# Kernel tuning notes

Hardware: AMD Instinct MI355X
Metric: run time of the kernel (lower is better)

## Reference

```python
import jax, jax.numpy as jnp
import numpy as np
import math

HIDDEN = 1024
HEADS = 16
HEAD_DIM = HIDDEN // HEADS
B, S = 2, 2048


def _xavier(key, shape):
    fan_in, fan_out = shape[1], shape[0]
    limit = math.sqrt(6.0 / (fan_in + fan_out))
    return jax.random.uniform(key, shape, jnp.float32, -limit, limit)


def setup_inputs() -> dict:
    key = jax.random.key(0)
    ks = jax.random.split(key, 5)
    x = jax.random.normal(ks[0], (B, S, HIDDEN), jnp.float32)
    # torch Linear stores weight as [out, in]; y = x @ W.T + b
    Wq = _xavier(ks[1], (HIDDEN, HIDDEN))
    Wk = _xavier(ks[2], (HIDDEN, HIDDEN))
    Wv = _xavier(ks[3], (HIDDEN, HIDDEN))
    Wo = _xavier(ks[4], (HIDDEN, HIDDEN))
    bq = jnp.zeros((HIDDEN,), jnp.float32)
    bk = jnp.zeros((HIDDEN,), jnp.float32)
    bv = jnp.zeros((HIDDEN,), jnp.float32)
    bo = jnp.zeros((HIDDEN,), jnp.float32)
    return {"x": x, "Wq": Wq, "bq": bq, "Wk": Wk, "bk": bk,
            "Wv": Wv, "bv": bv, "Wo": Wo, "bo": bo}


def reference(x, Wq, bq, Wk, bk, Wv, bv, Wo, bo):
    b, s, d = x.shape
    h, hd = HEADS, HEAD_DIM
    q = (x @ Wq.T + bq).reshape(b, s, h, hd).transpose(0, 2, 1, 3)  # [b,h,s,hd]
    k = (x @ Wk.T + bk).reshape(b, s, h, hd).transpose(0, 2, 1, 3)
    v = (x @ Wv.T + bv).reshape(b, s, h, hd).transpose(0, 2, 1, 3)
    scores = jnp.einsum('bhqd,bhkd->bhqk', q, k) / math.sqrt(hd)
    causal = jnp.tril(jnp.ones((s, s), bool))
    scores = jnp.where(causal, scores, -jnp.inf)
    attn = jax.nn.softmax(scores, axis=-1)
    out = jnp.einsum('bhqk,bhkd->bhqd', attn, v)  # [b,h,s,hd]
    out = out.transpose(0, 2, 1, 3).reshape(b, s, d)
    return out @ Wo.T + bo
```

## Files before the change

### kernel.cpp

```cpp
#include <hip/hip_runtime.h>
#include <hip/hip_bf16.h>


typedef __hip_bfloat16 bf16;
typedef __attribute__((ext_vector_type(8))) short short8;
typedef __attribute__((ext_vector_type(4))) short short4v;
typedef __attribute__((ext_vector_type(4))) float f32x4;
typedef __attribute__((ext_vector_type(2))) unsigned uint2v;
typedef __attribute__((ext_vector_type(4))) unsigned uint4v;

#define MFMA16(a, b, c) __builtin_amdgcn_mfma_f32_16x16x32_bf16((a), (b), (c), 0, 0, 0)

__device__ __forceinline__ void load_lds16(const void* g, void* l) {
  __builtin_amdgcn_global_load_lds(
      (const __attribute__((address_space(1))) void*)g,
      (__attribute__((address_space(3))) void*)l, 16, 0, 0);
}

#define QSCALE 0.18033688f

__global__ __launch_bounds__(256) void cvt_kernel(
    const float* __restrict__ x, const float* __restrict__ wq,
    const float* __restrict__ wk, const float* __restrict__ wv,
    const float* __restrict__ wo, bf16* __restrict__ xb,
    bf16* __restrict__ wcat) {
  const int bx = blockIdx.x;
  const float* src;
  bf16* dst;
  int ib;
  if (bx < 4096) { src = x; dst = xb; ib = bx; }
  else {
    const int wseg = (bx - 4096) >> 10;
    ib = (bx - 4096) & 1023;
    src = wseg == 0 ? wq : wseg == 1 ? wk : wseg == 2 ? wv : wo;
    dst = wcat + (size_t)wseg * 1048576;
  }
  const int i = (ib * 256 + threadIdx.x) * 4;
  const float4 v = *(const float4*)(src + i);
  short4v p;
  *(__hip_bfloat162*)&p = __float22bfloat162_rn(float2{v.x, v.y});
  *((__hip_bfloat162*)&p + 1) = __float22bfloat162_rn(float2{v.z, v.w});
  *(short4v*)(dst + i) = p;
}

__global__ __launch_bounds__(256) void qkv_kernel(
    const bf16* __restrict__ x, const bf16* __restrict__ Wcat,
    const float* __restrict__ bq, const float* __restrict__ bk,
    const float* __restrict__ bv, bf16* __restrict__ Qb,
    bf16* __restrict__ Kb, bf16* __restrict__ Vtg) {
  constexpr int K = 1024;
  __shared__ bf16 As[128 * 64];
  __shared__ bf16 Bs[128 * 64];
  const int t = threadIdx.x;
  const int lane = t & 63, w = t >> 6;
  const int quad = lane >> 4, r = lane & 15;
  const int bid = blockIdx.x;
  const int xcd = bid & 7, idx = bid >> 3;
  const int nloc = idx % 3, my = idx / 3;
  const int nx = xcd * 3 + nloc;
  const int m0 = my * 128;
  const int ncol = nx * 128;
  const int seg = ncol >> 10;
  const int n0 = ncol & 1023;
  const int wm = w >> 1, wn = w & 1;

  f32x4 acc[4][4] = {};

  for (int k0 = 0; k0 < K; k0 += 64) {
    __syncthreads();
#pragma unroll
    for (int p = 0; p < 4; ++p) {
      const int c = p * 256 + w * 64 + lane;
      const int row = c >> 3;
      const int scb = (c & 7) ^ (row & 7);
      load_lds16(x + (size_t)(m0 + row) * K + k0 + scb * 8, As + c * 8);
    }
#pragma unroll
    for (int p = 0; p < 4; ++p) {
      const int c = p * 256 + w * 64 + lane;
      const int row = c >> 3;
      const int scb = (c & 7) ^ (row & 7);
      load_lds16(Wcat + (size_t)(ncol + row) * K + k0 + scb * 8, Bs + c * 8);
    }
    __syncthreads();
    short8 af[4][2], bfr[4][2];
#pragma unroll
    for (int ks = 0; ks < 2; ++ks) {
#pragma unroll
      for (int i = 0; i < 4; ++i) {
        const int ra = wm * 64 + i * 16 + r;
        af[i][ks] = *(const short8*)(As + ra * 64 +
                                     (((ks * 4 + quad) ^ (ra & 7)) * 8));
        const int rb = wn * 64 + i * 16 + r;
        bfr[i][ks] = *(const short8*)(Bs + rb * 64 +
                                      (((ks * 4 + quad) ^ (rb & 7)) * 8));
      }
    }
#pragma unroll
    for (int ks = 0; ks < 2; ++ks)
#pragma unroll
      for (int i = 0; i < 4; ++i)
#pragma unroll
        for (int j = 0; j < 4; ++j)
          acc[i][j] = MFMA16(af[i][ks], bfr[j][ks], acc[i][j]);
  }

  const float* bias = seg == 0 ? bq : seg == 1 ? bk : bv;
  const float scale = seg == 0 ? QSCALE : 1.0f;
  bf16* dst01 = seg == 0 ? Qb : Kb;
#pragma unroll
  for (int i = 0; i < 4; ++i) {
    const int m = m0 + wm * 64 + i * 16 + quad * 4;
#pragma unroll
    for (int j = 0; j < 4; ++j) {
      const int nn = n0 + wn * 64 + j * 16 + r;
      const float bv_ = bias[nn];
      if (seg == 2) {
        short4v pk;
        *(__hip_bfloat162*)&pk = __float22bfloat162_rn(
            float2{acc[i][j][0] + bv_, acc[i][j][1] + bv_});
        *((__hip_bfloat162*)&pk + 1) = __float22bfloat162_rn(
            float2{acc[i][j][2] + bv_, acc[i][j][3] + bv_});
        *(short4v*)(Vtg + (size_t)nn * 4096 + m) = pk;
      } else {
#pragma unroll
        for (int g = 0; g < 4; ++g)
          dst01[(size_t)(m + g) * 1024 + nn] =
              __float2bfloat16((acc[i][j][g] + bv_) * scale);
      }
    }
  }
}

__global__ __launch_bounds__(256) void proj_kernel(const bf16* __restrict__ X,
                                                   const bf16* __restrict__ W,
                                                   const float* __restrict__ bias,
                                                   float* __restrict__ Y) {
  constexpr int K = 1024, N = 1024;
  __shared__ bf16 As[64 * 64];
  __shared__ bf16 Bs[128 * 64];
  const int t = threadIdx.x;
  const int lane = t & 63, w = t >> 6;
  const int quad = lane >> 4, r = lane & 15;
  const int bid = blockIdx.x;
  const int xcd = bid & 7, idx = bid >> 3;
  const int m0 = idx * 64, n0 = xcd * 128;
  const int wm = w >> 1, wn = w & 1;

  f32x4 acc[2][4] = {};

  for (int k0 = 0; k0 < K; k0 += 64) {
    __syncthreads();
#pragma unroll
    for (int p = 0; p < 2; ++p) {
      const int c = p * 256 + w * 64 + lane;
      const int row = c >> 3;
      const int scb = (c & 7) ^ (row & 7);
      load_lds16(X + (size_t)(m0 + row) * K + k0 + scb * 8, As + c * 8);
    }
#pragma unroll
    for (int p = 0; p < 4; ++p) {
      const int c = p * 256 + w * 64 + lane;
      const int row = c >> 3;
      const int scb = (c & 7) ^ (row & 7);
      load_lds16(W + (size_t)(n0 + row) * K + k0 + scb * 8, Bs + c * 8);
    }
    __syncthreads();
    short8 af[2][2], bfr[4][2];
#pragma unroll
    for (int ks = 0; ks < 2; ++ks) {
#pragma unroll
      for (int i = 0; i < 2; ++i) {
        const int ra = wm * 32 + i * 16 + r;
        af[i][ks] = *(const short8*)(As + ra * 64 +
                                     (((ks * 4 + quad) ^ (ra & 7)) * 8));
      }
#pragma unroll
      for (int j = 0; j < 4; ++j) {
        const int rb = wn * 64 + j * 16 + r;
        bfr[j][ks] = *(const short8*)(Bs + rb * 64 +
                                      (((ks * 4 + quad) ^ (rb & 7)) * 8));
      }
    }
#pragma unroll
    for (int ks = 0; ks < 2; ++ks)
#pragma unroll
      for (int i = 0; i < 2; ++i)
#pragma unroll
        for (int j = 0; j < 4; ++j)
          acc[i][j] = MFMA16(af[i][ks], bfr[j][ks], acc[i][j]);
  }
#pragma unroll
  for (int i = 0; i < 2; ++i) {
    const int m = m0 + wm * 32 + i * 16 + quad * 4;
#pragma unroll
    for (int j = 0; j < 4; ++j) {
      const int n = n0 + wn * 64 + j * 16 + r;
      const float bv = bias[n];
#pragma unroll
      for (int g = 0; g < 4; ++g)
        Y[(size_t)(m + g) * N + n] = acc[i][j][g] + bv;
    }
  }
}

__global__ __launch_bounds__(256, 4) void attn_kernel(const bf16* __restrict__ Qb,
                                                      const bf16* __restrict__ Kb,
                                                      const bf16* __restrict__ Vtg,
                                                      bf16* __restrict__ Ob) {
  const int bid = blockIdx.x;
  const int x = bid & 7, u = (bid >> 3) & 31, k = bid >> 8;
  const int g = x + 8 * k;
  const int h = g & 15, b = g >> 4;
  const int u8 = (u + 8) & 31;
  const int j = (k == 0) ? u : (k == 1) ? 31 - u : (k == 2) ? u8 : 31 - u8;
  const int T = j + 1;

  const int t = threadIdx.x;
  const int lane = t & 63, w = t >> 6;
  const int qs = w & 1, kst = w >> 1;
  const int quad = lane >> 4, r = lane & 15;

  __shared__ __align__(16) bf16 smem[16384];

  const bf16 *kg[2], *vg[2];
  int lofs[2];
#pragma unroll
  for (int p = 0; p < 2; ++p) {
    const int c = p * 256 + t;
    const int row = c >> 3, scb = (c & 7) ^ (row & 7);
    kg[p] = Kb + (size_t)(b * 2048 + row) * 1024 + h * 64 + scb * 8;
    vg[p] = Vtg + (size_t)(h * 64 + row) * 4096 + (size_t)b * 2048 + scb * 8;
    lofs[p] = c * 8;
  }

  auto stage_tile = [&](int tile, int slot) {
    bf16* const kd = smem + slot * 4096;
    bf16* const vd = smem + 8192 + slot * 4096;
#pragma unroll
    for (int p = 0; p < 2; ++p)
      load_lds16(kg[p] + (size_t)tile * 65536, kd + lofs[p]);
#pragma unroll
    for (int p = 0; p < 2; ++p)
      load_lds16(vg[p] + tile * 64, vd + lofs[p]);
  };

  short8 qf[2][2];
#pragma unroll
  for (int qfr = 0; qfr < 2; ++qfr)
#pragma unroll
    for (int ks = 0; ks < 2; ++ks)
      qf[qfr][ks] = *(const short8*)(
          Qb + (size_t)(b * 2048 + j * 64 + qs * 32 + qfr * 16 + r) * 1024 +
          h * 64 + ks * 32 + quad * 8);

  f32x4 o[4][2] = {};
  float lsum[2] = {0.f, 0.f};

  stage_tile(0, 0);
  for (int s = 0; s < T; ++s) {
    if (s + 1 < T) {
      stage_tile(s + 1, (s + 1) & 1);
      asm volatile("s_waitcnt vmcnt(4)" ::: "memory");
    } else {
      asm volatile("s_waitcnt vmcnt(0)" ::: "memory");
    }
    __builtin_amdgcn_s_barrier();
    __builtin_amdgcn_sched_barrier(0);

    const bf16* const ksb = smem + (s & 1) * 4096;
    const bf16* const vtb = smem + 8192 + (s & 1) * 4096;

    __builtin_amdgcn_s_setprio(1);
    short8 kf[2][2];
#pragma unroll
    for (int mt2 = 0; mt2 < 2; ++mt2) {
      const int krow = kst * 32 + mt2 * 16 + r;
#pragma unroll
      for (int ks = 0; ks < 2; ++ks)
        kf[mt2][ks] = *(const short8*)(ksb + krow * 64 +
                                       (((ks * 4 + quad) ^ (r & 7)) * 8));
    }
    f32x4 st[2][2] = {};
#pragma unroll
    for (int mt2 = 0; mt2 < 2; ++mt2)
#pragma unroll
      for (int qfr = 0; qfr < 2; ++qfr) {
        st[mt2][qfr] = MFMA16(kf[mt2][0], qf[qfr][0], st[mt2][qfr]);
        st[mt2][qfr] = MFMA16(kf[mt2][1], qf[qfr][1], st[mt2][qfr]);
      }
    if (s == T - 1) {
#pragma unroll
      for (int mt2 = 0; mt2 < 2; ++mt2)
#pragma unroll
        for (int qfr = 0; qfr < 2; ++qfr) {
          const int kb2 = s * 64 + kst * 32 + mt2 * 16 + quad * 4;
          const int qrow = j * 64 + qs * 32 + qfr * 16 + r;
#pragma unroll
          for (int g4 = 0; g4 < 4; ++g4)
            if (kb2 + g4 > qrow) st[mt2][qfr][g4] = -1e30f;
        }
    }
    unsigned cpk[2][2][2];
#pragma unroll
    for (int mt2 = 0; mt2 < 2; ++mt2)
#pragma unroll
      for (int qfr = 0; qfr < 2; ++qfr) {
        const float p0 = __builtin_amdgcn_exp2f(st[mt2][qfr][0]);
        const float p1 = __builtin_amdgcn_exp2f(st[mt2][qfr][1]);
        const float p2 = __builtin_amdgcn_exp2f(st[mt2][qfr][2]);
        const float p3 = __builtin_amdgcn_exp2f(st[mt2][qfr][3]);
        lsum[qfr] += (p0 + p1) + (p2 + p3);
        unsigned u0, u1;
        *(__hip_bfloat162*)&u0 = __float22bfloat162_rn(float2{p0, p1});
        *(__hip_bfloat162*)&u1 = __float22bfloat162_rn(float2{p2, p3});
        cpk[mt2][qfr][0] = u0;
        cpk[mt2][qfr][1] = u1;
      }
    short8 pf[2];
#pragma unroll
    for (int qfr = 0; qfr < 2; ++qfr) {
      unsigned br[4];
#pragma unroll
      for (int p2 = 0; p2 < 2; ++p2) {
        uint2v s32 = __builtin_amdgcn_permlane32_swap(
            cpk[0][qfr][p2], cpk[1][qfr][p2], false, false);
        uint2v s16 = __builtin_amdgcn_permlane16_swap(s32.x, s32.y,
                                                      false, false);
        br[p2] = s16.x; br[p2 + 2] = s16.y;
      }
      uint4v pv_; pv_.x = br[0]; pv_.y = br[1]; pv_.z = br[2]; pv_.w = br[3];
      pf[qfr] = __builtin_bit_cast(short8, pv_);
    }
#pragma unroll
    for (int mt = 0; mt < 4; ++mt) {
      const short8 vf = *(const short8*)(vtb + (mt * 16 + r) * 64 +
                                         (((kst * 4 + quad) ^ (r & 7)) * 8));
#pragma unroll
      for (int qfr = 0; qfr < 2; ++qfr)
        o[mt][qfr] = MFMA16(vf, pf[qfr], o[mt][qfr]);
    }
    __builtin_amdgcn_s_setprio(0);
    __builtin_amdgcn_sched_barrier(0);
    __builtin_amdgcn_s_barrier();
  }

#pragma unroll
  for (int qfr = 0; qfr < 2; ++qfr) {
    lsum[qfr] += __shfl_xor(lsum[qfr], 16);
    lsum[qfr] += __shfl_xor(lsum[qfr], 32);
  }
  __syncthreads();
  f32x4* const cb = (f32x4*)smem;
  float* const lb = (float*)(smem + 8192);
  if (kst == 1) {
#pragma unroll
    for (int mt = 0; mt < 4; ++mt)
#pragma unroll
      for (int qfr = 0; qfr < 2; ++qfr)
        cb[((qs * 2 + qfr) * 4 + mt) * 64 + lane] = o[mt][qfr];
#pragma unroll
    for (int qfr = 0; qfr < 2; ++qfr)
      lb[(qs * 2 + qfr) * 64 + lane] = lsum[qfr];
  }
  __syncthreads();
  if (kst == 0) {
    float inv[2];
#pragma unroll
    for (int qfr = 0; qfr < 2; ++qfr)
      inv[qfr] = 1.f / (lsum[qfr] + lb[(qs * 2 + qfr) * 64 + lane]);
#pragma unroll
    for (int mt = 0; mt < 4; ++mt)
#pragma unroll
      for (int qfr = 0; qfr < 2; ++qfr) {
        const f32x4 a = cb[((qs * 2 + qfr) * 4 + mt) * 64 + lane];
        short4v ph;
        *(__hip_bfloat162*)&ph = __float22bfloat162_rn(
            float2{(o[mt][qfr][0] + a[0]) * inv[qfr],
                   (o[mt][qfr][1] + a[1]) * inv[qfr]});
        *((__hip_bfloat162*)&ph + 1) = __float22bfloat162_rn(
            float2{(o[mt][qfr][2] + a[2]) * inv[qfr],
                   (o[mt][qfr][3] + a[3]) * inv[qfr]});
        *(short4v*)(Ob +
            (size_t)(b * 2048 + j * 64 + qs * 32 + qfr * 16 + r) * 1024 +
            h * 64 + mt * 16 + quad * 4) = ph;
      }
  }
}

extern "C" void kernel_launch(void* const* d_in, const int* in_sizes, int n_in,
                              void* d_out, int out_size, void* d_ws, size_t ws_size,
                              hipStream_t stream) {
  const float* x  = (const float*)d_in[0];
  const float* Wq = (const float*)d_in[1];
  const float* bq = (const float*)d_in[2];
  const float* Wk = (const float*)d_in[3];
  const float* bk = (const float*)d_in[4];
  const float* Wv = (const float*)d_in[5];
  const float* bv = (const float*)d_in[6];
  const float* Wo = (const float*)d_in[7];
  const float* bo = (const float*)d_in[8];
  float* out = (float*)d_out;

  bf16* xb   = (bf16*)d_ws;
  bf16* wcat = xb + (size_t)4096 * 1024;
  bf16* wob  = wcat + (size_t)3 * 1024 * 1024;
  bf16* Qb   = wcat + (size_t)4 * 1024 * 1024;
  bf16* Kb   = Qb  + (size_t)4096 * 1024;
  bf16* Vtg  = Kb  + (size_t)4096 * 1024;
  bf16* Ob   = Vtg + (size_t)4096 * 1024;
  const size_t need = ((size_t)4096 * 1024 * 5 + (size_t)1024 * 1024 * 4) * 2;
  if (ws_size < need) return;

  cvt_kernel<<<8192, 256, 0, stream>>>(x, Wq, Wk, Wv, Wo, xb, wcat);
  qkv_kernel<<<768, 256, 0, stream>>>(xb, wcat, bq, bk, bv, Qb, Kb, Vtg);
  attn_kernel<<<1024, 256, 0, stream>>>(Qb, Kb, Vtg, Ob);
  proj_kernel<<<512, 256, 0, stream>>>(Ob, wob, bo, out);
}
```

Baseline: 167.7 us.

## Restructure attention into single-wave blocks loading K/V straight to registers

The attention kernel drops its 4-wave blocks, which shared K/V tiles through double-buffered LDS and merged a split-K reduction at the end. It now launches 2048 one-wave blocks, each handling 32 query rows over the full 64-key tile. K and V fragments are loaded from global memory directly into registers with software double-buffering. This removes LDS staging, barriers and the cross-wave reduction, but each wave now fetches K/V on its own, which raises global/L2 traffic and register pressure.

```diff
diff --git a/kernel.cpp b/kernel.cpp
--- a/kernel.cpp
+++ b/kernel.cpp
@@ -204,86 +204,62 @@
   }
 }
 
-__global__ __launch_bounds__(256, 4) void attn_kernel(const bf16* __restrict__ Qb,
-                                                      const bf16* __restrict__ Kb,
-                                                      const bf16* __restrict__ Vtg,
-                                                      bf16* __restrict__ Ob) {
+__global__ __launch_bounds__(64, 2) void attn_kernel(const bf16* __restrict__ Qb,
+                                                     const bf16* __restrict__ Kb,
+                                                     const bf16* __restrict__ Vtg,
+                                                     bf16* __restrict__ Ob) {
   const int bid = blockIdx.x;
   const int x = bid & 7, u = (bid >> 3) & 31, k = bid >> 8;
-  const int g = x + 8 * k;
+  const int kk = k & 3, qh = k >> 2;
+  const int g = x + 8 * kk;
   const int h = g & 15, b = g >> 4;
   const int u8 = (u + 8) & 31;
-  const int j = (k == 0) ? u : (k == 1) ? 31 - u : (k == 2) ? u8 : 31 - u8;
+  const int j = (kk == 0) ? u : (kk == 1) ? 31 - u : (kk == 2) ? u8 : 31 - u8;
   const int T = j + 1;
 
-  const int t = threadIdx.x;
-  const int lane = t & 63, w = t >> 6;
-  const int qs = w & 1, kst = w >> 1;
+  const int lane = threadIdx.x & 63;
   const int quad = lane >> 4, r = lane & 15;
 
-  __shared__ __align__(16) bf16 smem[16384];
-
-  const bf16 *kg[2], *vg[2];
-  int lofs[2];
-#pragma unroll
-  for (int p = 0; p < 2; ++p) {
-    const int c = p * 256 + t;
-    const int row = c >> 3, scb = (c & 7) ^ (row & 7);
-    kg[p] = Kb + (size_t)(b * 2048 + row) * 1024 + h * 64 + scb * 8;
-    vg[p] = Vtg + (size_t)(h * 64 + row) * 4096 + (size_t)b * 2048 + scb * 8;
-    lofs[p] = c * 8;
-  }
-
-  auto stage_tile = [&](int tile, int slot) {
-    bf16* const kd = smem + slot * 4096;
-    bf16* const vd = smem + 8192 + slot * 4096;
-#pragma unroll
-    for (int p = 0; p < 2; ++p)
-      load_lds16(kg[p] + (size_t)tile * 65536, kd + lofs[p]);
-#pragma unroll
-    for (int p = 0; p < 2; ++p)
-      load_lds16(vg[p] + tile * 64, vd + lofs[p]);
+  const size_t kbase = (size_t)b * 2048 * 1024 + (size_t)r * 1024 +
+                       h * 64 + quad * 8;
+  const size_t vbase = (size_t)(h * 64 + r) * 4096 + (size_t)b * 2048 +
+                       quad * 8;
+
+  auto loadK = [&](int tile, short8 (&kf)[4][2]) {
+    const size_t tb = kbase + (size_t)tile * 65536;
+#pragma unroll
+    for (int mt2 = 0; mt2 < 4; ++mt2)
+#pragma unroll
+      for (int ks = 0; ks < 2; ++ks)
+        kf[mt2][ks] = *(const short8*)(Kb + tb + mt2 * 16384 + ks * 32);
   };
-
+  auto loadV = [&](int tile, short8 (&vf)[4][2]) {
+    const size_t tb = vbase + tile * 64;
+#pragma unroll
+    for (int mt = 0; mt < 4; ++mt)
+#pragma unroll
+      for (int ksl = 0; ksl < 2; ++ksl)
+        vf[mt][ksl] = *(const short8*)(Vtg + tb + mt * 65536 + ksl * 32);
+  };
+
+  const int qrow0 = j * 64 + qh * 32;
   short8 qf[2][2];
 #pragma unroll
   for (int qfr = 0; qfr < 2; ++qfr)
 #pragma unroll
     for (int ks = 0; ks < 2; ++ks)
       qf[qfr][ks] = *(const short8*)(
-          Qb + (size_t)(b * 2048 + j * 64 + qs * 32 + qfr * 16 + r) * 1024 +
+          Qb + (size_t)(b * 2048 + qrow0 + qfr * 16 + r) * 1024 +
           h * 64 + ks * 32 + quad * 8);
 
   f32x4 o[4][2] = {};
   float lsum[2] = {0.f, 0.f};
 
-  stage_tile(0, 0);
-  for (int s = 0; s < T; ++s) {
-    if (s + 1 < T) {
-      stage_tile(s + 1, (s + 1) & 1);
-      asm volatile("s_waitcnt vmcnt(4)" ::: "memory");
-    } else {
-      asm volatile("s_waitcnt vmcnt(0)" ::: "memory");
-    }
-    __builtin_amdgcn_s_barrier();
-    __builtin_amdgcn_sched_barrier(0);
-
-    const bf16* const ksb = smem + (s & 1) * 4096;
-    const bf16* const vtb = smem + 8192 + (s & 1) * 4096;
-
-    __builtin_amdgcn_s_setprio(1);
-    short8 kf[2][2];
-#pragma unroll
-    for (int mt2 = 0; mt2 < 2; ++mt2) {
-      const int krow = kst * 32 + mt2 * 16 + r;
-#pragma unroll
-      for (int ks = 0; ks < 2; ++ks)
-        kf[mt2][ks] = *(const short8*)(ksb + krow * 64 +
-                                       (((ks * 4 + quad) ^ (r & 7)) * 8));
-    }
-    f32x4 st[2][2] = {};
-#pragma unroll
-    for (int mt2 = 0; mt2 < 2; ++mt2)
+  auto compute = [&](const short8 (&kf)[4][2], const short8 (&vf)[4][2],
+                     int s) {
+    f32x4 st[4][2] = {};
+#pragma unroll
+    for (int mt2 = 0; mt2 < 4; ++mt2)
 #pragma unroll
       for (int qfr = 0; qfr < 2; ++qfr) {
         st[mt2][qfr] = MFMA16(kf[mt2][0], qf[qfr][0], st[mt2][qfr]);
@@ -291,19 +267,19 @@
       }
     if (s == T - 1) {
 #pragma unroll
-      for (int mt2 = 0; mt2 < 2; ++mt2)
+      for (int mt2 = 0; mt2 < 4; ++mt2)
 #pragma unroll
         for (int qfr = 0; qfr < 2; ++qfr) {
-          const int kb2 = s * 64 + kst * 32 + mt2 * 16 + quad * 4;
-          const int qrow = j * 64 + qs * 32 + qfr * 16 + r;
+          const int kb2 = s * 64 + mt2 * 16 + quad * 4;
+          const int qrow = qrow0 + qfr * 16 + r;
 #pragma unroll
           for (int g4 = 0; g4 < 4; ++g4)
             if (kb2 + g4 > qrow) st[mt2][qfr][g4] = -1e30f;
         }
     }
-    unsigned cpk[2][2][2];
-#pragma unroll
-    for (int mt2 = 0; mt2 < 2; ++mt2)
+    unsigned cpk[4][2][2];
+#pragma unroll
+    for (int mt2 = 0; mt2 < 4; ++mt2)
 #pragma unroll
       for (int qfr = 0; qfr < 2; ++qfr) {
         const float p0 = __builtin_amdgcn_exp2f(st[mt2][qfr][0]);
@@ -317,75 +293,65 @@
         cpk[mt2][qfr][0] = u0;
         cpk[mt2][qfr][1] = u1;
       }
-    short8 pf[2];
+    short8 pf[2][2];
+#pragma unroll
+    for (int ksl = 0; ksl < 2; ++ksl)
+#pragma unroll
+      for (int qfr = 0; qfr < 2; ++qfr) {
+        unsigned br[4];
+#pragma unroll
+        for (int p2 = 0; p2 < 2; ++p2) {
+          uint2v s32 = __builtin_amdgcn_permlane32_swap(
+              cpk[ksl * 2][qfr][p2], cpk[ksl * 2 + 1][qfr][p2], false, false);
+          uint2v s16 = __builtin_amdgcn_permlane16_swap(s32.x, s32.y,
+                                                        false, false);
+          br[p2] = s16.x; br[p2 + 2] = s16.y;
+        }
+        uint4v pv_; pv_.x = br[0]; pv_.y = br[1]; pv_.z = br[2]; pv_.w = br[3];
+        pf[ksl][qfr] = __builtin_bit_cast(short8, pv_);
+      }
+#pragma unroll
+    for (int mt = 0; mt < 4; ++mt)
+#pragma unroll
+      for (int ksl = 0; ksl < 2; ++ksl)
+#pragma unroll
+        for (int qfr = 0; qfr < 2; ++qfr)
+          o[mt][qfr] = MFMA16(vf[mt][ksl], pf[ksl][qfr], o[mt][qfr]);
+  };
+
+  short8 KA[4][2], KB[4][2], VA[4][2], VB[4][2];
+  loadK(0, KA);
+  loadV(0, VA);
+  int s = 0;
+  while (true) {
+    if (s + 1 < T) { loadK(s + 1, KB); loadV(s + 1, VB); }
+    compute(KA, VA, s);
+    if (++s == T) break;
+    if (s + 1 < T) { loadK(s + 1, KA); loadV(s + 1, VA); }
+    compute(KB, VB, s);
+    if (++s == T) break;
+  }
+
+  float inv[2];
+#pragma unroll
+  for (int qfr = 0; qfr < 2; ++qfr) {
+    float ls = lsum[qfr];
+    ls += __shfl_xor(ls, 16);
+    ls += __shfl_xor(ls, 32);
+    inv[qfr] = 1.f / ls;
+  }
+#pragma unroll
+  for (int mt = 0; mt < 4; ++mt)
 #pragma unroll
     for (int qfr = 0; qfr < 2; ++qfr) {
-      unsigned br[4];
-#pragma unroll
-      for (int p2 = 0; p2 < 2; ++p2) {
-        uint2v s32 = __builtin_amdgcn_permlane32_swap(
-            cpk[0][qfr][p2], cpk[1][qfr][p2], false, false);
-        uint2v s16 = __builtin_amdgcn_permlane16_swap(s32.x, s32.y,
-                                                      false, false);
-        br[p2] = s16.x; br[p2 + 2] = s16.y;
-      }
-      uint4v pv_; pv_.x = br[0]; pv_.y = br[1]; pv_.z = br[2]; pv_.w = br[3];
-      pf[qfr] = __builtin_bit_cast(short8, pv_);
-    }
-#pragma unroll
-    for (int mt = 0; mt < 4; ++mt) {
-      const short8 vf = *(const short8*)(vtb + (mt * 16 + r) * 64 +
-                                         (((kst * 4 + quad) ^ (r & 7)) * 8));
-#pragma unroll
-      for (int qfr = 0; qfr < 2; ++qfr)
-        o[mt][qfr] = MFMA16(vf, pf[qfr], o[mt][qfr]);
-    }
-    __builtin_amdgcn_s_setprio(0);
-    __builtin_amdgcn_sched_barrier(0);
-    __builtin_amdgcn_s_barrier();
-  }
-
-#pragma unroll
-  for (int qfr = 0; qfr < 2; ++qfr) {
-    lsum[qfr] += __shfl_xor(lsum[qfr], 16);
-    lsum[qfr] += __shfl_xor(lsum[qfr], 32);
-  }
-  __syncthreads();
-  f32x4* const cb = (f32x4*)smem;
-  float* const lb = (float*)(smem + 8192);
-  if (kst == 1) {
-#pragma unroll
-    for (int mt = 0; mt < 4; ++mt)
-#pragma unroll
-      for (int qfr = 0; qfr < 2; ++qfr)
-        cb[((qs * 2 + qfr) * 4 + mt) * 64 + lane] = o[mt][qfr];
-#pragma unroll
-    for (int qfr = 0; qfr < 2; ++qfr)
-      lb[(qs * 2 + qfr) * 64 + lane] = lsum[qfr];
-  }
-  __syncthreads();
-  if (kst == 0) {
-    float inv[2];
-#pragma unroll
-    for (int qfr = 0; qfr < 2; ++qfr)
-      inv[qfr] = 1.f / (lsum[qfr] + lb[(qs * 2 + qfr) * 64 + lane]);
-#pragma unroll
-    for (int mt = 0; mt < 4; ++mt)
-#pragma unroll
-      for (int qfr = 0; qfr < 2; ++qfr) {
-        const f32x4 a = cb[((qs * 2 + qfr) * 4 + mt) * 64 + lane];
-        short4v ph;
-        *(__hip_bfloat162*)&ph = __float22bfloat162_rn(
-            float2{(o[mt][qfr][0] + a[0]) * inv[qfr],
-                   (o[mt][qfr][1] + a[1]) * inv[qfr]});
-        *((__hip_bfloat162*)&ph + 1) = __float22bfloat162_rn(
-            float2{(o[mt][qfr][2] + a[2]) * inv[qfr],
-                   (o[mt][qfr][3] + a[3]) * inv[qfr]});
-        *(short4v*)(Ob +
-            (size_t)(b * 2048 + j * 64 + qs * 32 + qfr * 16 + r) * 1024 +
-            h * 64 + mt * 16 + quad * 4) = ph;
-      }
-  }
+      short4v ph;
+      *(__hip_bfloat162*)&ph = __float22bfloat162_rn(
+          float2{o[mt][qfr][0] * inv[qfr], o[mt][qfr][1] * inv[qfr]});
+      *((__hip_bfloat162*)&ph + 1) = __float22bfloat162_rn(
+          float2{o[mt][qfr][2] * inv[qfr], o[mt][qfr][3] * inv[qfr]});
+      *(short4v*)(Ob + (size_t)(b * 2048 + qrow0 + qfr * 16 + r) * 1024 +
+                  h * 64 + mt * 16 + quad * 4) = ph;
+    }
 }
 
 extern "C" void kernel_launch(void* const* d_in, const int* in_sizes, int n_in,
@@ -414,6 +380,6 @@
 
   cvt_kernel<<<8192, 256, 0, stream>>>(x, Wq, Wk, Wv, Wo, xb, wcat);
   qkv_kernel<<<768, 256, 0, stream>>>(xb, wcat, bq, bk, bv, Qb, Kb, Vtg);
-  attn_kernel<<<1024, 256, 0, stream>>>(Qb, Kb, Vtg, Ob);
+  attn_kernel<<<2048, 64, 0, stream>>>(Qb, Kb, Vtg, Ob);
   proj_kernel<<<512, 256, 0, stream>>>(Ob, wob, bo, out);
 }
```

Measured after the change: 209.0 us. +24.6%, slower.
